# Kernel optimization log

Measured on AMD Instinct MI355X. Metric: run time of the kernel, lower is better.

## Reference

```python
import jax, jax.numpy as jnp
import numpy as np
from jax.scipy.special import logsumexp

EPS = 0.1
MAX_ITER = 10
THRESH = 0.1


def setup_inputs() -> dict:
    key = jax.random.key(0)
    k1, k2 = jax.random.split(key)
    N, P, D = 16, 1024, 64
    y = jax.random.normal(k1, (N, P, D), dtype=jnp.float32)
    x = jax.random.normal(k2, (N, P, D), dtype=jnp.float32)
    return {"y": y, "x": x}


def reference(y, x):
    # Cost matrix |x_i - y_j|^2 summed over feature dim: (N, P1, P2)
    C = jnp.sum(jnp.abs(x[:, :, None, :] - y[:, None, :, :]) ** 2, axis=-1)
    N, P1, P2 = C.shape
    mu = jnp.full((N, P1), 1.0 / P1, dtype=C.dtype)
    nu = jnp.full((N, P2), 1.0 / P2, dtype=C.dtype)

    def M(u, v):
        # (-C + u_i + v_j) / eps
        return (-C + u[:, :, None] + v[:, None, :]) / EPS

    def body(carry, _):
        u, v, done = carry
        u_new = EPS * (jnp.log(mu + 1e-8) - logsumexp(M(u, v), axis=-1)) + u
        v_new = EPS * (jnp.log(nu + 1e-8) - logsumexp(M(u_new, v), axis=-2)) + v
        err = jnp.abs(u_new - u).sum(-1).mean()
        # emulate torch's early break: freeze updates once converged
        u2 = jnp.where(done, u, u_new)
        v2 = jnp.where(done, v, v_new)
        done2 = done | (err < THRESH)
        return (u2, v2, done2), None

    u0 = jnp.zeros_like(mu)
    v0 = jnp.zeros_like(nu)
    (u, v, _), _ = jax.lax.scan(body, (u0, v0, jnp.array(False)), None, length=MAX_ITER)
    pi = jnp.exp(M(u, v))  # transport plan (N, P1, P2)
    return pi
```

## Files before the change

kernel.cpp:

```cpp
#include <hip/hip_runtime.h>
#include <math.h>

#define NB 16
#define PP 1024
#define DD 64
#define MAX_ITER 10
#define RCH 16
#define NCH (PP / RCH)
#define NBLK (NB * NCH)

constexpr float EPSV    = 0.1f;
constexpr float SCALE_G = 20.0f;
constexpr float LOG2E   = 1.44269504088896340736f;
constexpr float LOG_MU  = -6.93146156597137f;
constexpr float THRESHV = 0.1f;

typedef short bf16x8 __attribute__((ext_vector_type(8)));
typedef float f32x16 __attribute__((ext_vector_type(16)));

__device__ __forceinline__ unsigned short f2bf(float f) {
  unsigned int u = __float_as_uint(f);
  return (unsigned short)((u + 0x7FFFu + ((u >> 16) & 1u)) >> 16);
}
__device__ __forceinline__ float bf2f(unsigned short h) {
  return __uint_as_float(((unsigned int)h) << 16);
}

__global__ __launch_bounds__(256) void prep_kernel(
    const float* __restrict__ x, const float* __restrict__ y,
    unsigned short* __restrict__ xh, unsigned short* __restrict__ xl,
    unsigned short* __restrict__ yh, unsigned short* __restrict__ yl,
    float* __restrict__ nxs, float* __restrict__ nys)
{
  const int sel = blockIdx.x >> 9;
  const int row = (blockIdx.x & 511) * 32 + (threadIdx.x >> 3);
  const int q   = threadIdx.x & 7;

  const float* src = sel ? y : x;
  unsigned short* H = sel ? yh : xh;
  unsigned short* L = sel ? yl : xl;
  float* N          = sel ? nys : nxs;

  const float* p = src + (size_t)row * DD + q * 8;
  float4 v0 = *(const float4*)(p);
  float4 v1 = *(const float4*)(p + 4);

  float f[8] = {v0.x, v0.y, v0.z, v0.w, v1.x, v1.y, v1.z, v1.w};
  float nrm = 0.f;
  unsigned short hb[8], lb[8];
  #pragma unroll
  for (int k = 0; k < 8; ++k) {
    nrm = fmaf(f[k], f[k], nrm);
    unsigned short h = f2bf(f[k]);
    float res = f[k] - bf2f(h);
    hb[k] = h; lb[k] = f2bf(res);
  }
  nrm += __shfl_xor(nrm, 1);
  nrm += __shfl_xor(nrm, 2);
  nrm += __shfl_xor(nrm, 4);
  if (q == 0) N[row] = 10.0f * nrm;

  uint4 ho, lo;
  ho.x = hb[0] | ((unsigned)hb[1] << 16); ho.y = hb[2] | ((unsigned)hb[3] << 16);
  ho.z = hb[4] | ((unsigned)hb[5] << 16); ho.w = hb[6] | ((unsigned)hb[7] << 16);
  lo.x = lb[0] | ((unsigned)lb[1] << 16); lo.y = lb[2] | ((unsigned)lb[3] << 16);
  lo.z = lb[4] | ((unsigned)lb[5] << 16); lo.w = lb[6] | ((unsigned)lb[7] << 16);
  *(uint4*)(H + (size_t)row * DD + q * 8) = ho;
  *(uint4*)(L + (size_t)row * DD + q * 8) = lo;
}

__global__ __launch_bounds__(256) void compute_c_mfma(
    const unsigned short* __restrict__ xh, const unsigned short* __restrict__ xl,
    const float* __restrict__ nxs,
    const unsigned short* __restrict__ yh, const unsigned short* __restrict__ yl,
    const float* __restrict__ nys,
    float* __restrict__ Cs)
{
  const int n   = blockIdx.x >> 8;
  const int ib  = (blockIdx.x >> 4) & 15;
  const int jb  = blockIdx.x & 15;
  const int tid = threadIdx.x;
  const int l   = tid & 63;
  const int w   = tid >> 6;
  const int ih  = w & 1, jh = w >> 1;

  __shared__ float nxv[64];
  if (tid < 64) nxv[tid] = nxs[n * PP + ib * 64 + tid];
  __syncthreads();

  const int jg  = n * PP + jb * 64 + 32 * jh + (l & 31);
  const float nyv = nys[jg];

  const int ko = 8 * (l >> 5);
  const size_t xrow = ((size_t)(n * PP + ib * 64 + 32 * ih + (l & 31))) * DD;
  const size_t yrow = ((size_t)jg) * DD;

  bf16x8 Xh0 = *(const bf16x8*)(xh + xrow + 0 * 16 + ko);
  bf16x8 Xh1 = *(const bf16x8*)(xh + xrow + 1 * 16 + ko);
  bf16x8 Xh2 = *(const bf16x8*)(xh + xrow + 2 * 16 + ko);
  bf16x8 Xh3 = *(const bf16x8*)(xh + xrow + 3 * 16 + ko);
  bf16x8 Xl0 = *(const bf16x8*)(xl + xrow + 0 * 16 + ko);
  bf16x8 Xl1 = *(const bf16x8*)(xl + xrow + 1 * 16 + ko);
  bf16x8 Xl2 = *(const bf16x8*)(xl + xrow + 2 * 16 + ko);
  bf16x8 Xl3 = *(const bf16x8*)(xl + xrow + 3 * 16 + ko);
  bf16x8 Yh0 = *(const bf16x8*)(yh + yrow + 0 * 16 + ko);
  bf16x8 Yh1 = *(const bf16x8*)(yh + yrow + 1 * 16 + ko);
  bf16x8 Yh2 = *(const bf16x8*)(yh + yrow + 2 * 16 + ko);
  bf16x8 Yh3 = *(const bf16x8*)(yh + yrow + 3 * 16 + ko);
  bf16x8 Yl0 = *(const bf16x8*)(yl + yrow + 0 * 16 + ko);
  bf16x8 Yl1 = *(const bf16x8*)(yl + yrow + 1 * 16 + ko);
  bf16x8 Yl2 = *(const bf16x8*)(yl + yrow + 2 * 16 + ko);
  bf16x8 Yl3 = *(const bf16x8*)(yl + yrow + 3 * 16 + ko);

  f32x16 acc;
  #pragma unroll
  for (int z = 0; z < 16; ++z) acc[z] = 0.f;
  acc = __builtin_amdgcn_mfma_f32_32x32x16_bf16(Xh0, Yh0, acc, 0, 0, 0);
  acc = __builtin_amdgcn_mfma_f32_32x32x16_bf16(Xh1, Yh1, acc, 0, 0, 0);
  acc = __builtin_amdgcn_mfma_f32_32x32x16_bf16(Xh2, Yh2, acc, 0, 0, 0);
  acc = __builtin_amdgcn_mfma_f32_32x32x16_bf16(Xh3, Yh3, acc, 0, 0, 0);
  acc = __builtin_amdgcn_mfma_f32_32x32x16_bf16(Xh0, Yl0, acc, 0, 0, 0);
  acc = __builtin_amdgcn_mfma_f32_32x32x16_bf16(Xh1, Yl1, acc, 0, 0, 0);
  acc = __builtin_amdgcn_mfma_f32_32x32x16_bf16(Xh2, Yl2, acc, 0, 0, 0);
  acc = __builtin_amdgcn_mfma_f32_32x32x16_bf16(Xh3, Yl3, acc, 0, 0, 0);
  acc = __builtin_amdgcn_mfma_f32_32x32x16_bf16(Xl0, Yh0, acc, 0, 0, 0);
  acc = __builtin_amdgcn_mfma_f32_32x32x16_bf16(Xl1, Yh1, acc, 0, 0, 0);
  acc = __builtin_amdgcn_mfma_f32_32x32x16_bf16(Xl2, Yh2, acc, 0, 0, 0);
  acc = __builtin_amdgcn_mfma_f32_32x32x16_bf16(Xl3, Yh3, acc, 0, 0, 0);

  const int irb  = 32 * ih + 4 * (l >> 5);
  const int jcol = jb * 64 + 32 * jh + (l & 31);
  #pragma unroll
  for (int r = 0; r < 16; ++r) {
    const int irel = irb + (r & 3) + 8 * (r >> 2);
    const size_t off = ((size_t)(n * PP + ib * 64 + irel)) * PP + jcol;
    Cs[off] = nxv[irel] + nyv - SCALE_G * acc[r];
  }
}

__global__ __launch_bounds__(256, 4) void iter_fused(
    const float* __restrict__ Cs, float* __restrict__ aG, const float* __restrict__ bG,
    float* __restrict__ pm, float* __restrict__ ps, float* __restrict__ errBlk,
    const int* __restrict__ doneFlags, int it)
{
  if (it > 0 && doneFlags[it - 1]) return;

  const int n   = blockIdx.x >> 6;
  const int rc  = blockIdx.x & (NCH - 1);
  const int tid = threadIdx.x;

  __shared__ float bb[PP];
  __shared__ float aArr[RCH];
  __shared__ float dsum[RCH];

  if (it == 0) {
    *(float4*)&bb[tid * 4] = make_float4(0.f, 0.f, 0.f, 0.f);
  } else {
    *(float4*)&bb[tid * 4] = *(const float4*)(bG + n * PP + tid * 4);
  }
  __syncthreads();

  const int r0  = tid >> 4;
  const int k   = tid & 15;
  const int row = n * PP + rc * RCH + r0;
  const float* crow = Cs + (size_t)row * PP + 4 * k;

  float4 tv[16];
  #pragma unroll
  for (int j = 0; j < 16; ++j) {
    float4 c4 = *(const float4*)(crow + 64 * j);
    float4 b4 = *(const float4*)&bb[4 * k + 64 * j];
    tv[j] = make_float4(b4.x - c4.x, b4.y - c4.y, b4.z - c4.z, b4.w - c4.w);
  }
  float m = -INFINITY;
  #pragma unroll
  for (int j = 0; j < 16; ++j)
    m = fmaxf(m, fmaxf(fmaxf(tv[j].x, tv[j].y), fmaxf(tv[j].z, tv[j].w)));
  #pragma unroll
  for (int mask = 8; mask; mask >>= 1) m = fmaxf(m, __shfl_xor(m, mask));

  float s = 0.f;
  #pragma unroll
  for (int j = 0; j < 16; ++j) {
    s += exp2f((tv[j].x - m) * LOG2E) + exp2f((tv[j].y - m) * LOG2E)
       + exp2f((tv[j].z - m) * LOG2E) + exp2f((tv[j].w - m) * LOG2E);
  }
  #pragma unroll
  for (int mask = 8; mask; mask >>= 1) s += __shfl_xor(s, mask);

  if (k == 0) {
    float aOld = (it == 0) ? 0.f : aG[row];
    float an = LOG_MU - (m + logf(s));
    aG[row]  = an;
    aArr[r0] = an;
    dsum[r0] = fabsf(an - aOld);
  }
  __syncthreads();
  if (tid == 0) {
    float e = 0.f;
    #pragma unroll
    for (int r = 0; r < RCH; ++r) e += dsum[r];
    errBlk[blockIdx.x] = e;
  }

  const int c0 = tid * 4;
  const float* cb = Cs + ((size_t)(n * PP + rc * RCH)) * PP + c0;

  float m0 = -INFINITY, m1 = -INFINITY, m2 = -INFINITY, m3 = -INFINITY;
  #pragma unroll
  for (int r = 0; r < RCH; ++r) {
    float ar = aArr[r];
    float4 c4 = *(const float4*)(cb + (size_t)r * PP);
    m0 = fmaxf(m0, ar - c4.x);
    m1 = fmaxf(m1, ar - c4.y);
    m2 = fmaxf(m2, ar - c4.z);
    m3 = fmaxf(m3, ar - c4.w);
  }
  float s0 = 0.f, s1 = 0.f, s2 = 0.f, s3 = 0.f;
  #pragma unroll
  for (int r = 0; r < RCH; ++r) {
    float ar = aArr[r];
    float4 c4 = *(const float4*)(cb + (size_t)r * PP);
    s0 += exp2f((ar - c4.x - m0) * LOG2E);
    s1 += exp2f((ar - c4.y - m1) * LOG2E);
    s2 += exp2f((ar - c4.z - m2) * LOG2E);
    s3 += exp2f((ar - c4.w - m3) * LOG2E);
  }
  size_t off = ((size_t)(n * NCH + rc)) * PP + c0;
  *(float4*)(pm + off) = make_float4(m0, m1, m2, m3);
  *(float4*)(ps + off) = make_float4(s0, s1, s2, s3);
}

__global__ __launch_bounds__(256) void v_combine(
    const float* __restrict__ pm, const float* __restrict__ ps,
    float* __restrict__ bG, const float* __restrict__ errBlk,
    int* __restrict__ doneFlags, int it)
{
  if (it > 0 && doneFlags[it - 1]) {
    if (blockIdx.x == 0 && threadIdx.x == 0) doneFlags[it] = 1;
    return;
  }
  const int col = blockIdx.x * 256 + threadIdx.x;
  const int n = col >> 10, j = col & (PP - 1);
  const float* pmn = pm + (size_t)n * NCH * PP + j;
  const float* psn = ps + (size_t)n * NCH * PP + j;

  float m = -INFINITY, s = 0.f;
  #pragma unroll 8
  for (int c = 0; c < NCH; ++c) {
    float mc = pmn[(size_t)c * PP];
    float sc = psn[(size_t)c * PP];
    float mn = fmaxf(m, mc);
    s = fmaf(s, exp2f((m - mn) * LOG2E), sc * exp2f((mc - mn) * LOG2E));
    m = mn;
  }
  bG[col] = LOG_MU - (m + logf(s));

  if (blockIdx.x == 0) {
    __shared__ float red[4];
    float loc = 0.f;
    for (int t = threadIdx.x; t < NBLK; t += 256) loc += errBlk[t];
    #pragma unroll
    for (int off = 32; off > 0; off >>= 1) loc += __shfl_xor(loc, off);
    if ((threadIdx.x & 63) == 0) red[threadIdx.x >> 6] = loc;
    __syncthreads();
    if (threadIdx.x == 0) {
      float tot = red[0] + red[1] + red[2] + red[3];
      float err = tot * (EPSV / (float)NB);
      doneFlags[it] = (err < THRESHV) ? 1 : 0;
    }
  }
}

__global__ __launch_bounds__(256) void pi_kernel(
    float* __restrict__ Cs, const float* __restrict__ a, const float* __restrict__ b)
{
  const int lane = threadIdx.x & 63;
  const int row  = (blockIdx.x << 2) + (threadIdx.x >> 6);
  const int n    = row >> 10;
  const float ai = a[row];
  float* crow = Cs + (size_t)row * PP;
  const float* bn = b + n * PP;
  #pragma unroll
  for (int kk = 0; kk < 4; ++kk) {
    float4 c4 = *(const float4*)(crow + lane * 4 + kk * 256);
    float4 b4 = *(const float4*)(bn   + lane * 4 + kk * 256);
    float4 r;
    r.x = exp2f((ai + b4.x - c4.x) * LOG2E);
    r.y = exp2f((ai + b4.y - c4.y) * LOG2E);
    r.z = exp2f((ai + b4.z - c4.z) * LOG2E);
    r.w = exp2f((ai + b4.w - c4.w) * LOG2E);
    *(float4*)(crow + lane * 4 + kk * 256) = r;
  }
}

extern "C" void kernel_launch(void* const* d_in, const int* in_sizes, int n_in,
                              void* d_out, int out_size, void* d_ws, size_t ws_size,
                              hipStream_t stream)
{
  const float* y = (const float*)d_in[0];
  const float* x = (const float*)d_in[1];

  float* Cs = (float*)d_out;

  const size_t NE = (size_t)NB * PP * DD;
  unsigned short* xh = (unsigned short*)d_ws;
  unsigned short* xl = xh + NE;
  unsigned short* yh = xl + NE;
  unsigned short* yl = yh + NE;
  float* pm = (float*)d_ws;
  float* ps = pm + (size_t)NB * NCH * PP;

  float* tail   = (float*)((char*)d_ws + 4 * NE * sizeof(unsigned short));
  float* nxs    = tail;
  float* nys    = nxs + NB * PP;
  float* aGl    = nys + NB * PP;
  float* bGl    = aGl + NB * PP;
  float* errBlk = bGl + NB * PP;
  int*   doneFl = (int*)(errBlk + NBLK);

  prep_kernel<<<1024, 256, 0, stream>>>(x, y, xh, xl, yh, yl, nxs, nys);
  compute_c_mfma<<<4096, 256, 0, stream>>>(xh, xl, nxs, yh, yl, nys, Cs);
  for (int it = 0; it < MAX_ITER; ++it) {
    iter_fused<<<NBLK, 256, 0, stream>>>(Cs, aGl, bGl, pm, ps, errBlk, doneFl, it);
    v_combine<<<NB * PP / 256, 256, 0, stream>>>(pm, ps, bGl, errBlk, doneFl, it);
  }
  pi_kernel<<<NB * PP / 4, 256, 0, stream>>>(Cs, aGl, bGl);
}
```

Baseline: 378.6 us.

## Recompute cost tile with MFMA in final plan kernel instead of reading C

The final transport-plan kernel no longer reads the stored cost matrix. It reruns prep (the workspace aliases pm/ps over the bf16 buffers, so they get overwritten) and recomputes each tile with split-bf16 MFMA, then applies exp directly. This removes a full 64MB read of C at the cost of an extra prep pass plus a second GEMM. The change also repacks the bf16 operands into an MFMA fragment-contiguous layout for coalesced 16-byte loads, and reorders block indices so the batch index varies fastest.

```diff
diff --git a/kernel.cpp b/kernel.cpp
--- a/kernel.cpp
+++ b/kernel.cpp
@@ -8,6 +8,7 @@
 #define RCH 16
 #define NCH (PP / RCH)
 #define NBLK (NB * NCH)
+#define CH (NB * PP)
 
 constexpr float EPSV    = 0.1f;
 constexpr float SCALE_G = 20.0f;
@@ -26,10 +27,14 @@
   return __uint_as_float(((unsigned int)h) << 16);
 }
 
+__device__ __forceinline__ const bf16x8* frag(const unsigned short* pk, int g, int q, int l) {
+  return (const bf16x8*)(pk + (((size_t)g * 4 + q) * 64 + l) * 8);
+}
+
 __global__ __launch_bounds__(256) void prep_kernel(
     const float* __restrict__ x, const float* __restrict__ y,
-    unsigned short* __restrict__ xh, unsigned short* __restrict__ xl,
-    unsigned short* __restrict__ yh, unsigned short* __restrict__ yl,
+    unsigned short* __restrict__ xhp, unsigned short* __restrict__ xlp,
+    unsigned short* __restrict__ yhp, unsigned short* __restrict__ ylp,
     float* __restrict__ nxs, float* __restrict__ nys)
 {
   const int sel = blockIdx.x >> 9;
@@ -37,8 +42,8 @@
   const int q   = threadIdx.x & 7;
 
   const float* src = sel ? y : x;
-  unsigned short* H = sel ? yh : xh;
-  unsigned short* L = sel ? yl : xl;
+  unsigned short* H = sel ? yhp : xhp;
+  unsigned short* L = sel ? ylp : xlp;
   float* N          = sel ? nys : nxs;
 
   const float* p = src + (size_t)row * DD + q * 8;
@@ -65,20 +70,24 @@
   ho.z = hb[4] | ((unsigned)hb[5] << 16); ho.w = hb[6] | ((unsigned)hb[7] << 16);
   lo.x = lb[0] | ((unsigned)lb[1] << 16); lo.y = lb[2] | ((unsigned)lb[3] << 16);
   lo.z = lb[4] | ((unsigned)lb[5] << 16); lo.w = lb[6] | ((unsigned)lb[7] << 16);
-  *(uint4*)(H + (size_t)row * DD + q * 8) = ho;
-  *(uint4*)(L + (size_t)row * DD + q * 8) = lo;
+
+  const int grp  = row >> 5;
+  const int lane = (row & 31) + 32 * (q & 1);
+  const size_t dst = (((size_t)grp * 4 + (q >> 1)) * 64 + lane) * 8;
+  *(uint4*)(H + dst) = ho;
+  *(uint4*)(L + dst) = lo;
 }
 
 __global__ __launch_bounds__(256) void compute_c_mfma(
-    const unsigned short* __restrict__ xh, const unsigned short* __restrict__ xl,
+    const unsigned short* __restrict__ xhp, const unsigned short* __restrict__ xlp,
     const float* __restrict__ nxs,
-    const unsigned short* __restrict__ yh, const unsigned short* __restrict__ yl,
+    const unsigned short* __restrict__ yhp, const unsigned short* __restrict__ ylp,
     const float* __restrict__ nys,
     float* __restrict__ Cs)
 {
-  const int n   = blockIdx.x >> 8;
+  const int n   = blockIdx.x & 15;
   const int ib  = (blockIdx.x >> 4) & 15;
-  const int jb  = blockIdx.x & 15;
+  const int jb  = blockIdx.x >> 8;
   const int tid = threadIdx.x;
   const int l   = tid & 63;
   const int w   = tid >> 6;
@@ -91,42 +100,22 @@
   const int jg  = n * PP + jb * 64 + 32 * jh + (l & 31);
   const float nyv = nys[jg];
 
-  const int ko = 8 * (l >> 5);
-  const size_t xrow = ((size_t)(n * PP + ib * 64 + 32 * ih + (l & 31))) * DD;
-  const size_t yrow = ((size_t)jg) * DD;
-
-  bf16x8 Xh0 = *(const bf16x8*)(xh + xrow + 0 * 16 + ko);
-  bf16x8 Xh1 = *(const bf16x8*)(xh + xrow + 1 * 16 + ko);
-  bf16x8 Xh2 = *(const bf16x8*)(xh + xrow + 2 * 16 + ko);
-  bf16x8 Xh3 = *(const bf16x8*)(xh + xrow + 3 * 16 + ko);
-  bf16x8 Xl0 = *(const bf16x8*)(xl + xrow + 0 * 16 + ko);
-  bf16x8 Xl1 = *(const bf16x8*)(xl + xrow + 1 * 16 + ko);
-  bf16x8 Xl2 = *(const bf16x8*)(xl + xrow + 2 * 16 + ko);
-  bf16x8 Xl3 = *(const bf16x8*)(xl + xrow + 3 * 16 + ko);
-  bf16x8 Yh0 = *(const bf16x8*)(yh + yrow + 0 * 16 + ko);
-  bf16x8 Yh1 = *(const bf16x8*)(yh + yrow + 1 * 16 + ko);
-  bf16x8 Yh2 = *(const bf16x8*)(yh + yrow + 2 * 16 + ko);
-  bf16x8 Yh3 = *(const bf16x8*)(yh + yrow + 3 * 16 + ko);
-  bf16x8 Yl0 = *(const bf16x8*)(yl + yrow + 0 * 16 + ko);
-  bf16x8 Yl1 = *(const bf16x8*)(yl + yrow + 1 * 16 + ko);
-  bf16x8 Yl2 = *(const bf16x8*)(yl + yrow + 2 * 16 + ko);
-  bf16x8 Yl3 = *(const bf16x8*)(yl + yrow + 3 * 16 + ko);
+  const int gX = n * 32 + ib * 2 + ih;
+  const int gY = n * 32 + jb * 2 + jh;
 
   f32x16 acc;
   #pragma unroll
   for (int z = 0; z < 16; ++z) acc[z] = 0.f;
-  acc = __builtin_amdgcn_mfma_f32_32x32x16_bf16(Xh0, Yh0, acc, 0, 0, 0);
-  acc = __builtin_amdgcn_mfma_f32_32x32x16_bf16(Xh1, Yh1, acc, 0, 0, 0);
-  acc = __builtin_amdgcn_mfma_f32_32x32x16_bf16(Xh2, Yh2, acc, 0, 0, 0);
-  acc = __builtin_amdgcn_mfma_f32_32x32x16_bf16(Xh3, Yh3, acc, 0, 0, 0);
-  acc = __builtin_amdgcn_mfma_f32_32x32x16_bf16(Xh0, Yl0, acc, 0, 0, 0);
-  acc = __builtin_amdgcn_mfma_f32_32x32x16_bf16(Xh1, Yl1, acc, 0, 0, 0);
-  acc = __builtin_amdgcn_mfma_f32_32x32x16_bf16(Xh2, Yl2, acc, 0, 0, 0);
-  acc = __builtin_amdgcn_mfma_f32_32x32x16_bf16(Xh3, Yl3, acc, 0, 0, 0);
-  acc = __builtin_amdgcn_mfma_f32_32x32x16_bf16(Xl0, Yh0, acc, 0, 0, 0);
-  acc = __builtin_amdgcn_mfma_f32_32x32x16_bf16(Xl1, Yh1, acc, 0, 0, 0);
-  acc = __builtin_amdgcn_mfma_f32_32x32x16_bf16(Xl2, Yh2, acc, 0, 0, 0);
-  acc = __builtin_amdgcn_mfma_f32_32x32x16_bf16(Xl3, Yh3, acc, 0, 0, 0);
+  #pragma unroll
+  for (int q = 0; q < 4; ++q) {
+    bf16x8 Xh = *frag(xhp, gX, q, l);
+    bf16x8 Xl = *frag(xlp, gX, q, l);
+    bf16x8 Yh = *frag(yhp, gY, q, l);
+    bf16x8 Yl = *frag(ylp, gY, q, l);
+    acc = __builtin_amdgcn_mfma_f32_32x32x16_bf16(Xh, Yh, acc, 0, 0, 0);
+    acc = __builtin_amdgcn_mfma_f32_32x32x16_bf16(Xh, Yl, acc, 0, 0, 0);
+    acc = __builtin_amdgcn_mfma_f32_32x32x16_bf16(Xl, Yh, acc, 0, 0, 0);
+  }
 
   const int irb  = 32 * ih + 4 * (l >> 5);
   const int jcol = jb * 64 + 32 * jh + (l & 31);
@@ -272,25 +261,55 @@
   }
 }
 
-__global__ __launch_bounds__(256) void pi_kernel(
-    float* __restrict__ Cs, const float* __restrict__ a, const float* __restrict__ b)
-{
-  const int lane = threadIdx.x & 63;
-  const int row  = (blockIdx.x << 2) + (threadIdx.x >> 6);
-  const int n    = row >> 10;
-  const float ai = a[row];
-  float* crow = Cs + (size_t)row * PP;
-  const float* bn = b + n * PP;
-  #pragma unroll
-  for (int kk = 0; kk < 4; ++kk) {
-    float4 c4 = *(const float4*)(crow + lane * 4 + kk * 256);
-    float4 b4 = *(const float4*)(bn   + lane * 4 + kk * 256);
-    float4 r;
-    r.x = exp2f((ai + b4.x - c4.x) * LOG2E);
-    r.y = exp2f((ai + b4.y - c4.y) * LOG2E);
-    r.z = exp2f((ai + b4.z - c4.z) * LOG2E);
-    r.w = exp2f((ai + b4.w - c4.w) * LOG2E);
-    *(float4*)(crow + lane * 4 + kk * 256) = r;
+__global__ __launch_bounds__(256) void pi_mfma(
+    const unsigned short* __restrict__ xhp, const unsigned short* __restrict__ xlp,
+    const unsigned short* __restrict__ yhp, const unsigned short* __restrict__ ylp,
+    const float* __restrict__ aG, const float* __restrict__ bG,
+    const float* __restrict__ nxs, const float* __restrict__ nys,
+    float* __restrict__ pi)
+{
+  const int n   = blockIdx.x & 15;
+  const int ib  = (blockIdx.x >> 4) & 15;
+  const int jb  = blockIdx.x >> 8;
+  const int tid = threadIdx.x;
+  const int l   = tid & 63;
+  const int w   = tid >> 6;
+  const int ih  = w & 1, jh = w >> 1;
+
+  __shared__ float atv[64];
+  if (tid < 64) {
+    int gi = n * PP + ib * 64 + tid;
+    atv[tid] = aG[gi] - nxs[gi];
+  }
+  __syncthreads();
+
+  const int jg  = n * PP + jb * 64 + 32 * jh + (l & 31);
+  const float btv = bG[jg] - nys[jg];
+
+  const int gX = n * 32 + ib * 2 + ih;
+  const int gY = n * 32 + jb * 2 + jh;
+
+  f32x16 acc;
+  #pragma unroll
+  for (int z = 0; z < 16; ++z) acc[z] = 0.f;
+  #pragma unroll
+  for (int q = 0; q < 4; ++q) {
+    bf16x8 Xh = *frag(xhp, gX, q, l);
+    bf16x8 Xl = *frag(xlp, gX, q, l);
+    bf16x8 Yh = *frag(yhp, gY, q, l);
+    bf16x8 Yl = *frag(ylp, gY, q, l);
+    acc = __builtin_amdgcn_mfma_f32_32x32x16_bf16(Xh, Yh, acc, 0, 0, 0);
+    acc = __builtin_amdgcn_mfma_f32_32x32x16_bf16(Xh, Yl, acc, 0, 0, 0);
+    acc = __builtin_amdgcn_mfma_f32_32x32x16_bf16(Xl, Yh, acc, 0, 0, 0);
+  }
+
+  const int irb  = 32 * ih + 4 * (l >> 5);
+  const int jcol = jb * 64 + 32 * jh + (l & 31);
+  #pragma unroll
+  for (int r = 0; r < 16; ++r) {
+    const int irel = irb + (r & 3) + 8 * (r >> 2);
+    const size_t off = ((size_t)(n * PP + ib * 64 + irel)) * PP + jcol;
+    pi[off] = exp2f((atv[irel] + btv + SCALE_G * acc[r]) * LOG2E);
   }
 }
 
@@ -304,26 +323,27 @@
   float* Cs = (float*)d_out;
 
   const size_t NE = (size_t)NB * PP * DD;
-  unsigned short* xh = (unsigned short*)d_ws;
-  unsigned short* xl = xh + NE;
-  unsigned short* yh = xl + NE;
-  unsigned short* yl = yh + NE;
+  unsigned short* xhp = (unsigned short*)d_ws;
+  unsigned short* xlp = xhp + NE;
+  unsigned short* yhp = xlp + NE;
+  unsigned short* ylp = yhp + NE;
   float* pm = (float*)d_ws;
   float* ps = pm + (size_t)NB * NCH * PP;
 
   float* tail   = (float*)((char*)d_ws + 4 * NE * sizeof(unsigned short));
   float* nxs    = tail;
-  float* nys    = nxs + NB * PP;
-  float* aGl    = nys + NB * PP;
-  float* bGl    = aGl + NB * PP;
-  float* errBlk = bGl + NB * PP;
+  float* nys    = nxs + CH;
+  float* aG     = nys + CH;
+  float* bG     = aG + CH;
+  float* errBlk = bG + CH;
   int*   doneFl = (int*)(errBlk + NBLK);
 
-  prep_kernel<<<1024, 256, 0, stream>>>(x, y, xh, xl, yh, yl, nxs, nys);
-  compute_c_mfma<<<4096, 256, 0, stream>>>(xh, xl, nxs, yh, yl, nys, Cs);
+  prep_kernel<<<1024, 256, 0, stream>>>(x, y, xhp, xlp, yhp, ylp, nxs, nys);
+  compute_c_mfma<<<4096, 256, 0, stream>>>(xhp, xlp, nxs, yhp, ylp, nys, Cs);
   for (int it = 0; it < MAX_ITER; ++it) {
-    iter_fused<<<NBLK, 256, 0, stream>>>(Cs, aGl, bGl, pm, ps, errBlk, doneFl, it);
-    v_combine<<<NB * PP / 256, 256, 0, stream>>>(pm, ps, bGl, errBlk, doneFl, it);
-  }
-  pi_kernel<<<NB * PP / 4, 256, 0, stream>>>(Cs, aGl, bGl);
-}
+    iter_fused<<<NBLK, 256, 0, stream>>>(Cs, aG, bG, pm, ps, errBlk, doneFl, it);
+    v_combine<<<NB * PP / 256, 256, 0, stream>>>(pm, ps, bG, errBlk, doneFl, it);
+  }
+  prep_kernel<<<1024, 256, 0, stream>>>(x, y, xhp, xlp, yhp, ylp, nxs, nys);
+  pi_mfma<<<4096, 256, 0, stream>>>(xhp, xlp, yhp, ylp, aG, bG, nxs, nys, Cs);
+}
```

Result: faster. 366.7 us (-3.2%).
